# Optimization experiments

Measured on AMD Instinct MI355X. Metric: run time of the kernel, lower is better.

Reference implementation:

```python
import jax, jax.numpy as jnp
import numpy as np

N_CHANNELS = 1024
N_HEADS = 16
SEQ = 2048
BATCH = 2


def setup_inputs() -> dict:
    key = jax.random.key(0)
    k1, k2, k3 = jax.random.split(key, 3)
    x = jax.random.normal(k1, (BATCH, SEQ, N_CHANNELS), dtype=jnp.float32)
    qkv_w = jax.random.normal(k2, (3 * N_CHANNELS, N_CHANNELS), dtype=jnp.float32) * 0.02
    qkv_b = jnp.zeros((3 * N_CHANNELS,), dtype=jnp.float32)
    proj_w = jax.random.normal(k3, (N_CHANNELS, N_CHANNELS), dtype=jnp.float32) * 0.02
    proj_b = jnp.zeros((N_CHANNELS,), dtype=jnp.float32)
    return {"x": x, "qkv_w": qkv_w, "qkv_b": qkv_b, "proj_w": proj_w, "proj_b": proj_b}


def reference(x, qkv_w, qkv_b, proj_w, proj_b):
    bs, t, c = x.shape
    h = N_HEADS
    hd = c // h
    scale = hd ** (-0.5)
    # qkv projection: torch Linear is x @ W^T + b
    qkv = x @ qkv_w.T + qkv_b  # [B, T, 3C]
    qkv = qkv.reshape(bs, t, 3, h, hd)
    q, k, v = qkv[:, :, 0], qkv[:, :, 1], qkv[:, :, 2]  # each [B, T, H, hd]
    logits = jnp.einsum('bthc,bshc->bhts', q, k) * scale  # [B, H, T, T]
    # causal mask: log(tril(ones)) -> 0 below diag, -inf above
    causal = jnp.tril(jnp.ones((t, t), dtype=bool))
    logits = jnp.where(causal[None, None], logits, -jnp.inf)
    attn = jax.nn.softmax(logits, axis=-1)
    out = jnp.einsum('bhts,bshc->bthc', attn, v).reshape(bs, t, c)
    out = out @ proj_w.T + proj_b
    return out
```

## Files before the change

kernel.cpp:

```cpp
#include <hip/hip_runtime.h>

typedef __bf16 bf16x8 __attribute__((ext_vector_type(8)));
typedef float f32x4 __attribute__((ext_vector_type(4)));

__device__ inline ushort f2bf(float f) {
    unsigned u = __builtin_bit_cast(unsigned, f);
    unsigned r = (u + 0x7FFFu + ((u >> 16) & 1u)) >> 16;
    return (ushort)r;
}
__device__ inline float bf2f(ushort u) {
    unsigned x = ((unsigned)u) << 16;
    return __builtin_bit_cast(float, x);
}
__device__ inline uint4 pack8(const float* f) {
    uint4 r;
    r.x = (unsigned)f2bf(f[0]) | ((unsigned)f2bf(f[1]) << 16);
    r.y = (unsigned)f2bf(f[2]) | ((unsigned)f2bf(f[3]) << 16);
    r.z = (unsigned)f2bf(f[4]) | ((unsigned)f2bf(f[5]) << 16);
    r.w = (unsigned)f2bf(f[6]) | ((unsigned)f2bf(f[7]) << 16);
    return r;
}

#define MFMA_BF16(a, b, c) __builtin_amdgcn_mfma_f32_16x16x32_bf16(a, b, c, 0, 0, 0)
#define GLDS(g, l) __builtin_amdgcn_global_load_lds( \
    (const __attribute__((address_space(1))) void*)(g), \
    (__attribute__((address_space(3))) void*)(l), 16, 0, 0)

#define QSCALE 0.18033688011112042f

__global__ __launch_bounds__(256) void convert3(
    const float* __restrict__ s0, ushort* __restrict__ d0,
    const float* __restrict__ s1, ushort* __restrict__ d1,
    const float* __restrict__ s2, ushort* __restrict__ d2)
{
    const int i = blockIdx.x * 256 + threadIdx.x;
    const float* s; ushort* d; int off;
    if (i < 524288)      { s = s0; d = d0; off = i; }
    else if (i < 917504) { s = s1; d = d1; off = i - 524288; }
    else                 { s = s2; d = d2; off = i - 917504; }
    const float4* f = (const float4*)s + off * 2;
    float fa[8];
    *(float4*)&fa[0] = f[0];
    *(float4*)&fa[4] = f[1];
    ((uint4*)d)[off] = pack8(fa);
}

__global__ __launch_bounds__(256) void gemm_qkv(
    const ushort* __restrict__ A, const ushort* __restrict__ B,
    const float* __restrict__ bias,
    ushort* __restrict__ outQ, ushort* __restrict__ outK, ushort* __restrict__ outV,
    int N, int K)
{
    __shared__ __align__(16) ushort SMEM[32768];

    const int tid = threadIdx.x;
    const int w = tid >> 6;
    const int lane = tid & 63;
    const int l15 = lane & 15;
    const int quad = lane >> 4;
    const int srow = lane >> 3;

    const int bid = blockIdx.x + (blockIdx.y << 5);
    const int xcd = bid & 7;
    const int local = bid >> 3;
    const int mi_t = local & 7;
    const int ni_t = local >> 3;
    const int m0 = ((xcd & 3) * 8 + mi_t) * 128;
    const int n0 = (((xcd >> 2) * 12) + ni_t) * 128;
    const int wr = (w & 1) * 64;
    const int wc = (w >> 1) * 64;

    auto stage = [&](int k0, int buf) {
        ushort* As = SMEM + buf * 16384;
        ushort* Bs = As + 8192;
#pragma unroll
        for (int j = 0; j < 4; j++) {
            const int r0 = w * 32 + j * 8;
            const int row = r0 + srow;
            const int gcol = ((lane & 7) ^ (row & 7)) * 8;
            GLDS(A + (size_t)(m0 + row) * K + k0 + gcol, As + r0 * 64);
            GLDS(B + (size_t)(n0 + row) * K + k0 + gcol, Bs + r0 * 64);
        }
    };

    f32x4 acc[4][4] = {};

    stage(0, 0);
    __syncthreads();

    for (int k0 = 0; k0 < K; k0 += 64) {
        const int cur = (k0 >> 6) & 1;
        if (k0 + 64 < K) stage(k0 + 64, cur ^ 1);

        const ushort* As = SMEM + cur * 16384;
        const ushort* Bs = As + 8192;
        bf16x8 af[4][2], bf[4][2];
#pragma unroll
        for (int i = 0; i < 4; i++)
#pragma unroll
            for (int kk = 0; kk < 2; kk++) {
                const int ra = wr + i * 16 + l15;
                const int rb = wc + i * 16 + l15;
                af[i][kk] = *(const bf16x8*)&As[ra * 64 + (((kk * 4 + quad) ^ (ra & 7)) * 8)];
                bf[i][kk] = *(const bf16x8*)&Bs[rb * 64 + (((kk * 4 + quad) ^ (rb & 7)) * 8)];
            }
#pragma unroll
        for (int kk = 0; kk < 2; kk++)
#pragma unroll
            for (int mi = 0; mi < 4; mi++)
#pragma unroll
                for (int ni = 0; ni < 4; ni++)
                    acc[mi][ni] = MFMA_BF16(af[mi][kk], bf[ni][kk], acc[mi][ni]);
        __syncthreads();
    }

    const int which = n0 >> 10;
    ushort* Ct = SMEM;
    if (which == 2) {
#pragma unroll
        for (int mi = 0; mi < 4; mi++)
#pragma unroll
            for (int ni = 0; ni < 4; ni++)
#pragma unroll
                for (int r = 0; r < 4; r++) {
                    const int m_loc = wr + mi * 16 + quad * 4 + r;
                    const int n_loc = wc + ni * 16 + l15;
                    Ct[n_loc * 136 + m_loc] =
                        f2bf(acc[mi][ni][r] + bias[n0 + n_loc]);
                }
        __syncthreads();
        const int b = m0 >> 11;
#pragma unroll
        for (int i = 0; i < 8; i++) {
            const int vi = tid + i * 256;
            const int n_loc = vi >> 4, mblk = vi & 15;
            const uint4 val = *(const uint4*)&Ct[n_loc * 136 + mblk * 8];
            const int t = (m0 & 2047) + mblk * 8;
            const int c = (n0 + n_loc) & 1023;
            const int h = c >> 6, d = c & 63;
            *(uint4*)&outV[((size_t)(b * 16 + h) * 64 + d) * 2048 + t] = val;
        }
    } else {
        const float qs = (which == 0) ? QSCALE : 1.0f;
#pragma unroll
        for (int mi = 0; mi < 4; mi++)
#pragma unroll
            for (int ni = 0; ni < 4; ni++)
#pragma unroll
                for (int r = 0; r < 4; r++) {
                    const int m_loc = wr + mi * 16 + quad * 4 + r;
                    const int n_loc = wc + ni * 16 + l15;
                    Ct[m_loc * 136 + n_loc] =
                        f2bf((acc[mi][ni][r] + bias[n0 + n_loc]) * qs);
                }
        __syncthreads();
        ushort* outP = (which == 0) ? outQ : outK;
        const int hb = (n0 & 1023) >> 6;
        const int b = m0 >> 11;
#pragma unroll
        for (int i = 0; i < 8; i++) {
            const int vi = tid + i * 256;
            const int m_loc = vi >> 4, u = vi & 15;
            const uint4 val = *(const uint4*)&Ct[m_loc * 136 + u * 8];
            const int t = (m0 & 2047) + m_loc;
            const int h = hb + (u >> 3);
            const int d8 = (u & 7) * 8;
            *(uint4*)&outP[((size_t)(b * 16 + h)) * 131072 + (size_t)t * 64 + d8] = val;
        }
    }
}

__global__ __launch_bounds__(256) void gemm_proj(
    const ushort* __restrict__ A, const ushort* __restrict__ B,
    const float* __restrict__ bias, float* __restrict__ outD)
{
    const int N = 1024, K = 1024;
    __shared__ __align__(16) ushort SMEM[24576];

    const int tid = threadIdx.x;
    const int w = tid >> 6;
    const int lane = tid & 63;
    const int l15 = lane & 15;
    const int quad = lane >> 4;
    const int srow = lane >> 3;

    const int bid = blockIdx.x + (blockIdx.y << 6);
    const int nb = (bid & 7) * 64 + (bid >> 3);
    const int m0 = (nb >> 3) * 64;
    const int n0 = (nb & 7) * 128;
    const int wr = (w & 1) * 32;
    const int wc = (w >> 1) * 64;

    auto stage = [&](int k0, int buf) {
        ushort* As = SMEM + buf * 12288;
        ushort* Bs = As + 4096;
#pragma unroll
        for (int j = 0; j < 2; j++) {
            const int r0 = w * 16 + j * 8;
            const int row = r0 + srow;
            const int gcol = ((lane & 7) ^ (row & 7)) * 8;
            GLDS(A + (size_t)(m0 + row) * K + k0 + gcol, As + r0 * 64);
        }
#pragma unroll
        for (int j = 0; j < 4; j++) {
            const int r0 = w * 32 + j * 8;
            const int row = r0 + srow;
            const int gcol = ((lane & 7) ^ (row & 7)) * 8;
            GLDS(B + (size_t)(n0 + row) * K + k0 + gcol, Bs + r0 * 64);
        }
    };

    f32x4 acc[2][4] = {};

    stage(0, 0);
    __syncthreads();

    for (int k0 = 0; k0 < K; k0 += 64) {
        const int cur = (k0 >> 6) & 1;
        if (k0 + 64 < K) stage(k0 + 64, cur ^ 1);

        const ushort* As = SMEM + cur * 12288;
        const ushort* Bs = As + 4096;
        bf16x8 af[2][2], bf[4][2];
#pragma unroll
        for (int kk = 0; kk < 2; kk++) {
#pragma unroll
            for (int mi = 0; mi < 2; mi++) {
                const int ra = wr + mi * 16 + l15;
                af[mi][kk] = *(const bf16x8*)&As[ra * 64 + (((kk * 4 + quad) ^ (ra & 7)) * 8)];
            }
#pragma unroll
            for (int ni = 0; ni < 4; ni++) {
                const int rb = wc + ni * 16 + l15;
                bf[ni][kk] = *(const bf16x8*)&Bs[rb * 64 + (((kk * 4 + quad) ^ (rb & 7)) * 8)];
            }
        }
#pragma unroll
        for (int kk = 0; kk < 2; kk++)
#pragma unroll
            for (int mi = 0; mi < 2; mi++)
#pragma unroll
                for (int ni = 0; ni < 4; ni++)
                    acc[mi][ni] = MFMA_BF16(af[mi][kk], bf[ni][kk], acc[mi][ni]);
        __syncthreads();
    }

    float* Cf = (float*)SMEM;
#pragma unroll
    for (int cch = 0; cch < 2; cch++) {
        __syncthreads();
        if ((wc >> 6) == cch) {
#pragma unroll
            for (int mi = 0; mi < 2; mi++)
#pragma unroll
                for (int ni = 0; ni < 4; ni++)
#pragma unroll
                    for (int r = 0; r < 4; r++) {
                        const int m_loc = wr + mi * 16 + quad * 4 + r;
                        const int nl = ni * 16 + l15;
                        Cf[m_loc * 68 + nl] = acc[mi][ni][r] + bias[n0 + cch * 64 + nl];
                    }
        }
        __syncthreads();
#pragma unroll
        for (int i = 0; i < 4; i++) {
            const int vi = tid + i * 256;
            const int m_loc = vi >> 4, u = vi & 15;
            const float4 val = *(const float4*)&Cf[m_loc * 68 + u * 4];
            *(float4*)&outD[(size_t)(m0 + m_loc) * N + n0 + cch * 64 + u * 4] = val;
        }
    }
}

__global__ __launch_bounds__(256) void attn_split(
    const ushort* __restrict__ Q, const ushort* __restrict__ K,
    const ushort* __restrict__ Vt, ushort* __restrict__ O,
    ushort* __restrict__ Opart, float* __restrict__ Lpart)
{
    __shared__ __align__(16) ushort KV[2][2][64 * 64];
    __shared__ __align__(16) __bf16 Ps[4][16 * 64];

    const int bh = blockIdx.x;
    const int y = blockIdx.y;
    int qt, k0, k1, chunk, split;
    if (y < 48) {
        qt = 31 - (y >> 1); chunk = y & 1; split = 1;
        const int n = qt + 1, h = (n + 1) >> 1;
        k0 = chunk ? h : 0; k1 = chunk ? n : h;
    } else {
        qt = 55 - y; chunk = 0; split = 0; k0 = 0; k1 = qt + 1;
    }
    const int q0 = qt * 64;
    const int tid = threadIdx.x;
    const int w = tid >> 6;
    const int lane = tid & 63;
    const int l15 = lane & 15;
    const int quad = lane >> 4;

    auto stage = [&](int kt, int b) {
        const int t0 = kt * 64;
#pragma unroll
        for (int j = 0; j < 2; j++) {
            const int r0 = w * 16 + j * 8;
            const int row = r0 + (lane >> 3);
            const int gcol = ((lane & 7) ^ (row & 7)) * 8;
            GLDS(K + ((size_t)bh * 2048 + t0 + row) * 64 + gcol, &KV[b][0][r0 * 64]);
            GLDS(Vt + ((size_t)bh * 64 + row) * 2048 + t0 + gcol, &KV[b][1][r0 * 64]);
        }
    };

    const ushort* qbase = Q + ((size_t)bh * 2048 + q0 + w * 16 + l15) * 64;
    bf16x8 qf0 = *(const bf16x8*)(qbase + quad * 8);
    bf16x8 qf1 = *(const bf16x8*)(qbase + 32 + quad * 8);

    bf16x8 ones;
#pragma unroll
    for (int j = 0; j < 8; j++) ones[j] = (__bf16)1.0f;

    f32x4 oacc[4] = {};
    f32x4 lacc = {};

    stage(k0, 0);

    for (int kt = k0; kt < k1; kt++) {
        __syncthreads();
        if (kt + 1 < k1) stage(kt + 1, (kt + 1 - k0) & 1);

        const ushort* Ks = &KV[(kt - k0) & 1][0][0];
        const ushort* Vs = &KV[(kt - k0) & 1][1][0];
        const int t0 = kt * 64;

        f32x4 sacc[4] = {};
#pragma unroll
        for (int cb = 0; cb < 4; cb++) {
            const int rr = cb * 16 + l15;
            bf16x8 b0 = *(const bf16x8*)&Ks[rr * 64 + ((quad ^ (rr & 7)) * 8)];
            bf16x8 b1 = *(const bf16x8*)&Ks[rr * 64 + (((4 + quad) ^ (rr & 7)) * 8)];
            sacc[cb] = MFMA_BF16(qf0, b0, sacc[cb]);
            sacc[cb] = MFMA_BF16(qf1, b1, sacc[cb]);
        }

        __bf16* pw = &Ps[w][0];
        __builtin_amdgcn_wave_barrier();
#pragma unroll
        for (int cb = 0; cb < 4; cb++)
#pragma unroll
            for (int r = 0; r < 4; r++) {
                float x = sacc[cb][r];
                if (kt == qt) {
                    const int col = t0 + cb * 16 + l15;
                    const int row = q0 + w * 16 + quad * 4 + r;
                    if (col > row) x = -1e30f;
                }
                const int prow = quad * 4 + r;
                const int unit = cb * 2 + (l15 >> 3);
                pw[prow * 64 + ((unit ^ (prow & 7)) * 8) + (l15 & 7)] =
                    (__bf16)__builtin_exp2f(x);
            }
        __builtin_amdgcn_s_waitcnt(0xC07F);
        __builtin_amdgcn_wave_barrier();

#pragma unroll
        for (int kc = 0; kc < 2; kc++) {
            bf16x8 afr = *(const bf16x8*)&pw[l15 * 64 + (((kc * 4 + quad) ^ (l15 & 7)) * 8)];
#pragma unroll
            for (int cb = 0; cb < 4; cb++) {
                const int rr = cb * 16 + l15;
                bf16x8 bfr = *(const bf16x8*)&Vs[rr * 64 + (((kc * 4 + quad) ^ (rr & 7)) * 8)];
                oacc[cb] = MFMA_BF16(afr, bfr, oacc[cb]);
            }
            lacc = MFMA_BF16(afr, ones, lacc);
        }
    }

    if (!split) {
        const int b = bh >> 4, h = bh & 15;
#pragma unroll
        for (int r = 0; r < 4; r++) {
            const float inv = 1.0f / lacc[r];
            const int row = q0 + w * 16 + quad * 4 + r;
#pragma unroll
            for (int cb = 0; cb < 4; cb++) {
                const int col = h * 64 + cb * 16 + l15;
                O[((size_t)b * 2048 + row) * 1024 + col] = f2bf(oacc[cb][r] * inv);
            }
        }
    } else {
        const size_t slot2 = ((size_t)bh * 24 + (qt - 8)) * 2 + chunk;
        if (l15 == 0) {
#pragma unroll
            for (int r = 0; r < 4; r++)
                Lpart[slot2 * 64 + w * 16 + quad * 4 + r] = lacc[r];
        }
        __bf16* pw = &Ps[w][0];
        __builtin_amdgcn_wave_barrier();
#pragma unroll
        for (int cb = 0; cb < 4; cb++)
#pragma unroll
            for (int r = 0; r < 4; r++) {
                const int prow = quad * 4 + r;
                const int unit = cb * 2 + (l15 >> 3);
                pw[prow * 64 + ((unit ^ (prow & 7)) * 8) + (l15 & 7)] =
                    (__bf16)oacc[cb][r];
            }
        __builtin_amdgcn_s_waitcnt(0xC07F);
        __builtin_amdgcn_wave_barrier();
        const int r = lane >> 2, u = lane & 3;
        const int p0 = (2 * u) ^ (r & 7), p1 = (2 * u + 1) ^ (r & 7);
        const uint4 a = *(const uint4*)&pw[r * 64 + p0 * 8];
        const uint4 b = *(const uint4*)&pw[r * 64 + p1 * 8];
        ushort* dst = Opart + slot2 * 4096 + (w * 16 + r) * 64 + u * 16;
        *(uint4*)dst = a;
        *(uint4*)(dst + 8) = b;
    }
}

__global__ __launch_bounds__(256) void attn_combine(
    const ushort* __restrict__ Opart, const float* __restrict__ Lpart,
    ushort* __restrict__ O)
{
    const int bh = blockIdx.x;
    const int qt = 8 + blockIdx.y;
    const int tid = threadIdx.x;
    const int row = tid >> 2;
    const int cg = (tid & 3) * 16;
    const size_t s = ((size_t)bh * 24 + (qt - 8)) * 2;
    const ushort* p0 = Opart + s * 4096 + row * 64 + cg;
    const ushort* p1 = p0 + 4096;
    const float inv = 1.0f / (Lpart[s * 64 + row] + Lpart[(s + 1) * 64 + row]);
    const int b = bh >> 4, h = bh & 15;
    ushort* dst = O + ((size_t)b * 2048 + qt * 64 + row) * 1024 + h * 64 + cg;
    ushort out[16];
#pragma unroll
    for (int v = 0; v < 2; v++) {
        uint4 a = *(const uint4*)(p0 + v * 8);
        uint4 c = *(const uint4*)(p1 + v * 8);
        const ushort* ua = (const ushort*)&a;
        const ushort* uc = (const ushort*)&c;
#pragma unroll
        for (int j = 0; j < 8; j++)
            out[v * 8 + j] = f2bf((bf2f(ua[j]) + bf2f(uc[j])) * inv);
    }
    *(uint4*)dst = *(uint4*)&out[0];
    *(uint4*)(dst + 8) = *(uint4*)&out[8];
}

extern "C" void kernel_launch(void* const* d_in, const int* in_sizes, int n_in,
                              void* d_out, int out_size, void* d_ws, size_t ws_size,
                              hipStream_t stream) {
    const float* x      = (const float*)d_in[0];
    const float* qkv_w  = (const float*)d_in[1];
    const float* qkv_b  = (const float*)d_in[2];
    const float* proj_w = (const float*)d_in[3];
    const float* proj_b = (const float*)d_in[4];

    ushort* XbOb  = (ushort*)d_ws + 16;
    ushort* Wqkv  = XbOb + 4194304;
    ushort* Wproj = Wqkv + 3145728;
    ushort* Qb    = Wproj + 1048576;
    ushort* Kb    = Qb + 4194304;
    ushort* Vt    = Kb + 4194304;
    ushort* Opart = Vt + 4194304;
    float*  Lpart = (float*)(Opart + 6291456);

    convert3<<<4096, 256, 0, stream>>>(x, XbOb, qkv_w, Wqkv, proj_w, Wproj);
    gemm_qkv<<<dim3(32, 24), 256, 0, stream>>>(XbOb, Wqkv, qkv_b,
                                               Qb, Kb, Vt, 3072, 1024);
    attn_split<<<dim3(32, 56), 256, 0, stream>>>(Qb, Kb, Vt, XbOb, Opart, Lpart);
    attn_combine<<<dim3(32, 24), 256, 0, stream>>>(Opart, Lpart, XbOb);
    gemm_proj<<<dim3(64, 8), 256, 0, stream>>>(XbOb, Wproj, proj_b, (float*)d_out);
}
```

Before: 190.2 us.

## Keep attention probabilities in registers via transposed QK MFMA and permlane swaps

The QK^T MFMA operands are swapped so each lane holds transposed scores, and the probabilities are packed to bf16 with v_cvt_pk_bf16_f32. They are then rearranged into the PV A-operand layout with permlane32/permlane16 swaps instead of a round trip through the per-wave LDS P buffer. This removes LDS stores and loads, the waitcnt and the wave barriers from the inner attention loop. The risk is that the lane mapping of the swaps must exactly match the MFMA operand layout, and the causal mask indexing was rewritten to follow the transposed layout.

```diff
diff --git a/kernel.cpp b/kernel.cpp
--- a/kernel.cpp
+++ b/kernel.cpp
@@ -18,6 +18,11 @@
     r.y = (unsigned)f2bf(f[2]) | ((unsigned)f2bf(f[3]) << 16);
     r.z = (unsigned)f2bf(f[4]) | ((unsigned)f2bf(f[5]) << 16);
     r.w = (unsigned)f2bf(f[6]) | ((unsigned)f2bf(f[7]) << 16);
+    return r;
+}
+__device__ inline unsigned cvtpk_bf16(float lo, float hi) {
+    unsigned r;
+    asm("v_cvt_pk_bf16_f32 %0, %1, %2" : "=v"(r) : "v"(lo), "v"(hi));
     return r;
 }
 
@@ -320,6 +325,8 @@
     f32x4 oacc[4] = {};
     f32x4 lacc = {};
 
+    const int qg = q0 + w * 16 + l15;
+
     stage(k0, 0);
 
     for (int kt = k0; kt < k1; kt++) {
@@ -336,40 +343,43 @@
             const int rr = cb * 16 + l15;
             bf16x8 b0 = *(const bf16x8*)&Ks[rr * 64 + ((quad ^ (rr & 7)) * 8)];
             bf16x8 b1 = *(const bf16x8*)&Ks[rr * 64 + (((4 + quad) ^ (rr & 7)) * 8)];
-            sacc[cb] = MFMA_BF16(qf0, b0, sacc[cb]);
-            sacc[cb] = MFMA_BF16(qf1, b1, sacc[cb]);
-        }
-
-        __bf16* pw = &Ps[w][0];
-        __builtin_amdgcn_wave_barrier();
-#pragma unroll
-        for (int cb = 0; cb < 4; cb++)
+            sacc[cb] = MFMA_BF16(b0, qf0, sacc[cb]);
+            sacc[cb] = MFMA_BF16(b1, qf1, sacc[cb]);
+        }
+
+        unsigned pk[4][2];
+        const int kbase = t0 + quad * 4;
+#pragma unroll
+        for (int cb = 0; cb < 4; cb++) {
+            float p[4];
 #pragma unroll
             for (int r = 0; r < 4; r++) {
                 float x = sacc[cb][r];
-                if (kt == qt) {
-                    const int col = t0 + cb * 16 + l15;
-                    const int row = q0 + w * 16 + quad * 4 + r;
-                    if (col > row) x = -1e30f;
-                }
-                const int prow = quad * 4 + r;
-                const int unit = cb * 2 + (l15 >> 3);
-                pw[prow * 64 + ((unit ^ (prow & 7)) * 8) + (l15 & 7)] =
-                    (__bf16)__builtin_exp2f(x);
-            }
-        __builtin_amdgcn_s_waitcnt(0xC07F);
-        __builtin_amdgcn_wave_barrier();
+                if (kt == qt && (kbase + cb * 16 + r > qg)) x = -1e30f;
+                p[r] = __builtin_exp2f(x);
+            }
+            pk[cb][0] = cvtpk_bf16(p[0], p[1]);
+            pk[cb][1] = cvtpk_bf16(p[2], p[3]);
+        }
 
 #pragma unroll
         for (int kc = 0; kc < 2; kc++) {
-            bf16x8 afr = *(const bf16x8*)&pw[l15 * 64 + (((kc * 4 + quad) ^ (l15 & 7)) * 8)];
+            unsigned x0 = pk[kc * 2][0], y0 = pk[kc * 2 + 1][0];
+            unsigned x1 = pk[kc * 2][1], y1 = pk[kc * 2 + 1][1];
+            asm("v_permlane32_swap_b32 %0, %1" : "+v"(x0), "+v"(y0));
+            asm("v_permlane16_swap_b32 %0, %1" : "+v"(x0), "+v"(y0));
+            asm("v_permlane32_swap_b32 %0, %1" : "+v"(x1), "+v"(y1));
+            asm("v_permlane16_swap_b32 %0, %1" : "+v"(x1), "+v"(y1));
+            uint4 av;
+            av.x = x0; av.y = x1; av.z = y0; av.w = y1;
+            bf16x8 af = __builtin_bit_cast(bf16x8, av);
 #pragma unroll
             for (int cb = 0; cb < 4; cb++) {
                 const int rr = cb * 16 + l15;
                 bf16x8 bfr = *(const bf16x8*)&Vs[rr * 64 + (((kc * 4 + quad) ^ (rr & 7)) * 8)];
-                oacc[cb] = MFMA_BF16(afr, bfr, oacc[cb]);
-            }
-            lacc = MFMA_BF16(afr, ones, lacc);
+                oacc[cb] = MFMA_BF16(af, bfr, oacc[cb]);
+            }
+            lacc = MFMA_BF16(af, ones, lacc);
         }
     }
 
```

New measurement: 187.7 us. Within noise of the previous version (-1.3%).
